# Kernel optimization log

Measured on AMD Instinct MI355X. Metric: run time of the kernel, lower is better.

## Reference

```python
import jax, jax.numpy as jnp
import numpy as np

EPS = 1e-12  # matches torch.nn.functional.normalize default eps


def setup_inputs() -> dict:
    key = jax.random.key(0)
    k1, k2 = jax.random.split(key)
    text_emb = jax.random.normal(k1, (64, 512), dtype=jnp.float32)
    spot_embs = jax.random.normal(k2, (500000, 512), dtype=jnp.float32)
    return {"text_emb": text_emb, "spot_embs": spot_embs, "top_k": 10}


def _l2_normalize(x):
    # F.normalize: x / max(||x||_2, eps)
    n = jnp.linalg.norm(x, axis=-1, keepdims=True)
    return x / jnp.maximum(n, EPS)


def reference(text_emb, spot_embs, top_k):
    t = _l2_normalize(text_emb)          # [B, D]
    s = _l2_normalize(spot_embs)         # [N, D]
    scores = jnp.einsum('bd,nd->bn', t, s)  # [B, N] cosine similarity
    _, indices = jax.lax.top_k(scores, top_k)  # [B, top_k]
    return scores, indices
```

## Files before the change

### kernel.cpp

```cpp
#include <hip/hip_runtime.h>
#include <hip/hip_bf16.h>

#define B_TEXT 64
#define D_DIM  512
#define TOPK   10
#define TILE_N 128
#define BK     64
#define LDA    (BK + 8)
#define CH     16

typedef short bf16x8 __attribute__((ext_vector_type(8)));
typedef float f32x4  __attribute__((ext_vector_type(4)));

__device__ __forceinline__ unsigned short f2bf(float x) {
    unsigned u = __float_as_uint(x);
    u += 0x7fffu + ((u >> 16) & 1u);
    return (unsigned short)(u >> 16);
}
__device__ __forceinline__ float bf2f(unsigned short h) {
    return __uint_as_float(((unsigned)h) << 16);
}

__global__ void prep_text(const float* __restrict__ T, unsigned short* __restrict__ tHi,
                          unsigned short* __restrict__ tLo) {
    int b = blockIdx.x;
    int lane = threadIdx.x;
    const float* row = T + b * D_DIM;
    float4 a = *(const float4*)(row + lane * 4);
    float4 c = *(const float4*)(row + 256 + lane * 4);
    float p = a.x*a.x + a.y*a.y + a.z*a.z + a.w*a.w
            + c.x*c.x + c.y*c.y + c.z*c.z + c.w*c.w;
    #pragma unroll
    for (int off = 1; off < 64; off <<= 1) p += __shfl_xor(p, off);
    float inv = 1.0f / fmaxf(sqrtf(p), 1e-12f);
    float v[8] = {a.x, a.y, a.z, a.w, c.x, c.y, c.z, c.w};
    #pragma unroll
    for (int j = 0; j < 8; ++j) {
        float y = v[j] * inv;
        unsigned short hi = f2bf(y);
        unsigned short lo = f2bf(y - bf2f(hi));
        int col = (j < 4) ? (lane * 4 + j) : (256 + lane * 4 + (j - 4));
        tHi[b * D_DIM + col] = hi;
        tLo[b * D_DIM + col] = lo;
    }
}

__global__ __launch_bounds__(256, 2) void gemm_scores(
    const float* __restrict__ S, const unsigned short* __restrict__ tHi,
    const unsigned short* __restrict__ tLo, float* __restrict__ out, int N) {

    __shared__ unsigned short As_hi[B_TEXT][LDA];
    __shared__ unsigned short As_lo[B_TEXT][LDA];
    __shared__ unsigned short Bs_hi[TILE_N][LDA];
    __shared__ unsigned short Bs_lo[TILE_N][LDA];
    __shared__ float s_ss[TILE_N];

    const int tid  = threadIdx.x;
    const int n0   = blockIdx.x * TILE_N;
    const int lane = tid & 63;
    const int w    = tid >> 6;
    const int l15  = lane & 15;
    const int quad = lane >> 4;

    if (tid < TILE_N) s_ss[tid] = 0.0f;

    f32x4 acc[4][2];
    const f32x4 zf = {0.f, 0.f, 0.f, 0.f};
    #pragma unroll
    for (int i = 0; i < 4; ++i)
        #pragma unroll
        for (int j = 0; j < 2; ++j) acc[i][j] = zf;

    const int arow = tid >> 2;
    const int akq  = (tid & 3) << 4;

    for (int kc = 0; kc < D_DIM; kc += BK) {
        __syncthreads();
        {
            const uint4* ph = (const uint4*)(tHi + arow * D_DIM + kc + akq);
            const uint4* pl = (const uint4*)(tLo + arow * D_DIM + kc + akq);
            uint4 h0 = ph[0], h1 = ph[1];
            uint4 l0 = pl[0], l1 = pl[1];
            *(uint4*)&As_hi[arow][akq]     = h0;
            *(uint4*)&As_hi[arow][akq + 8] = h1;
            *(uint4*)&As_lo[arow][akq]     = l0;
            *(uint4*)&As_lo[arow][akq + 8] = l1;
        }
        #pragma unroll
        for (int i = 0; i < 8; ++i) {
            int flat = i * 1024 + tid * 4;
            int r = flat >> 6;
            int k = flat & 63;
            float4 v;
            if (n0 + r < N) v = *(const float4*)(S + (size_t)(n0 + r) * D_DIM + kc + k);
            else            v = make_float4(0.f, 0.f, 0.f, 0.f);
            ushort4 h, l;
            h.x = f2bf(v.x); l.x = f2bf(v.x - bf2f(h.x));
            h.y = f2bf(v.y); l.y = f2bf(v.y - bf2f(h.y));
            h.z = f2bf(v.z); l.z = f2bf(v.z - bf2f(h.z));
            h.w = f2bf(v.w); l.w = f2bf(v.w - bf2f(h.w));
            *(ushort4*)&Bs_hi[r][k] = h;
            *(ushort4*)&Bs_lo[r][k] = l;
            float p = v.x*v.x + v.y*v.y + v.z*v.z + v.w*v.w;
            p += __shfl_xor(p, 1);
            p += __shfl_xor(p, 2);
            p += __shfl_xor(p, 4);
            p += __shfl_xor(p, 8);
            if ((tid & 15) == 0) s_ss[r] += p;
        }
        __syncthreads();
        #pragma unroll
        for (int ks = 0; ks < 2; ++ks) {
            const int off = ks * 32 + quad * 8;
            bf16x8 ah[4], al[4], bh[2], bl[2];
            #pragma unroll
            for (int mt = 0; mt < 4; ++mt) {
                int m = mt * 16 + l15;
                ah[mt] = *(const bf16x8*)&As_hi[m][off];
                al[mt] = *(const bf16x8*)&As_lo[m][off];
            }
            #pragma unroll
            for (int nt = 0; nt < 2; ++nt) {
                int nl = w * 32 + nt * 16 + l15;
                bh[nt] = *(const bf16x8*)&Bs_hi[nl][off];
                bl[nt] = *(const bf16x8*)&Bs_lo[nl][off];
            }
            #pragma unroll
            for (int mt = 0; mt < 4; ++mt)
                #pragma unroll
                for (int nt = 0; nt < 2; ++nt) {
                    acc[mt][nt] = __builtin_amdgcn_mfma_f32_16x16x32_bf16(ah[mt], bh[nt], acc[mt][nt], 0, 0, 0);
                    acc[mt][nt] = __builtin_amdgcn_mfma_f32_16x16x32_bf16(ah[mt], bl[nt], acc[mt][nt], 0, 0, 0);
                    acc[mt][nt] = __builtin_amdgcn_mfma_f32_16x16x32_bf16(al[mt], bh[nt], acc[mt][nt], 0, 0, 0);
                }
        }
    }
    __syncthreads();
    #pragma unroll
    for (int nt = 0; nt < 2; ++nt) {
        int nl = w * 32 + nt * 16 + l15;
        int n  = n0 + nl;
        if (n >= N) continue;
        float inv = 1.0f / fmaxf(sqrtf(s_ss[nl]), 1e-12f);
        #pragma unroll
        for (int mt = 0; mt < 4; ++mt) {
            #pragma unroll
            for (int r = 0; r < 4; ++r) {
                int m = mt * 16 + quad * 4 + r;
                out[(size_t)m * N + n] = acc[mt][nt][r] * inv;
            }
        }
    }
}

__global__ __launch_bounds__(256) void topk_part(
    const float* __restrict__ scores, float* __restrict__ cs, int* __restrict__ ci, int N) {
    const int b = blockIdx.y;
    const int c = blockIdx.x;
    const int t = threadIdx.x;
    const int chunk = (N + CH - 1) / CH;
    const int base  = c * chunk;
    const float* row = scores + (size_t)b * N;

    float ts[TOPK]; int ti[TOPK];
    #pragma unroll
    for (int j = 0; j < TOPK; ++j) { ts[j] = -3.4e38f; ti[j] = 0x7fffffff; }

    for (int e = t; e < chunk; e += 256) {
        int n = base + e;
        if (n >= N) break;
        float v = row[n];
        if (v > ts[TOPK - 1]) {
            float cv = v; int cidx = n;
            #pragma unroll
            for (int j = 0; j < TOPK; ++j) {
                bool g = (cv > ts[j]);
                float ns = g ? cv : ts[j]; int ni = g ? cidx : ti[j];
                cv = g ? ts[j] : cv; cidx = g ? ti[j] : cidx;
                ts[j] = ns; ti[j] = ni;
            }
        }
    }

    __shared__ float all_s[256][TOPK];
    __shared__ int   all_i[256][TOPK];
    #pragma unroll
    for (int j = 0; j < TOPK; ++j) { all_s[t][j] = ts[j]; all_i[t][j] = ti[j]; }

    __shared__ float rs[256]; __shared__ int ri[256]; __shared__ int rt[256];
    int ptr = 0;
    __syncthreads();

    for (int round = 0; round < TOPK; ++round) {
        rs[t] = (ptr < TOPK) ? all_s[t][ptr] : -3.4e38f;
        ri[t] = (ptr < TOPK) ? all_i[t][ptr] : 0x7fffffff;
        rt[t] = t;
        __syncthreads();
        for (int s = 128; s > 0; s >>= 1) {
            if (t < s) {
                bool take = (rs[t + s] > rs[t]) ||
                            (rs[t + s] == rs[t] && ri[t + s] < ri[t]);
                if (take) { rs[t] = rs[t + s]; ri[t] = ri[t + s]; rt[t] = rt[t + s]; }
            }
            __syncthreads();
        }
        if (t == 0) {
            cs[((size_t)b * CH + c) * TOPK + round] = rs[0];
            ci[((size_t)b * CH + c) * TOPK + round] = ri[0];
        }
        if (t == rt[0]) ++ptr;
        __syncthreads();
    }
}

__global__ void topk_final(const float* __restrict__ cs, const int* __restrict__ ci,
                           float* __restrict__ outIdx) {
    const int b = blockIdx.x;
    const int t = threadIdx.x;
    __shared__ float fs[CH * TOPK];
    __shared__ int   fi[CH * TOPK];
    for (int j = t; j < CH * TOPK; j += 64) {
        fs[j] = cs[(size_t)b * CH * TOPK + j];
        fi[j] = ci[(size_t)b * CH * TOPK + j];
    }
    __syncthreads();
    if (t == 0) {
        float ts[TOPK]; int ti[TOPK];
        #pragma unroll
        for (int j = 0; j < TOPK; ++j) { ts[j] = -3.4e38f; ti[j] = 0x7fffffff; }
        for (int e = 0; e < CH * TOPK; ++e) {
            float cv = fs[e]; int cidx = fi[e];
            if (cv > ts[TOPK - 1] || (cv == ts[TOPK - 1] && cidx < ti[TOPK - 1])) {
                #pragma unroll
                for (int j = 0; j < TOPK; ++j) {
                    bool g = (cv > ts[j]) || (cv == ts[j] && cidx < ti[j]);
                    float ns = g ? cv : ts[j]; int ni = g ? cidx : ti[j];
                    cv = g ? ts[j] : cv; cidx = g ? ti[j] : cidx;
                    ts[j] = ns; ti[j] = ni;
                }
            }
        }
        #pragma unroll
        for (int j = 0; j < TOPK; ++j) outIdx[b * TOPK + j] = (float)ti[j];
    }
}

extern "C" void kernel_launch(void* const* d_in, const int* in_sizes, int n_in,
                              void* d_out, int out_size, void* d_ws, size_t ws_size,
                              hipStream_t stream) {
    const float* T = (const float*)d_in[0];
    const float* S = (const float*)d_in[1];
    const int N = in_sizes[1] / D_DIM;
    float* out = (float*)d_out;

    unsigned short* tHi = (unsigned short*)d_ws;
    unsigned short* tLo = tHi + B_TEXT * D_DIM;
    float* cs = (float*)(tLo + B_TEXT * D_DIM);
    int*   ci = (int*)(cs + B_TEXT * CH * TOPK);

    prep_text<<<B_TEXT, 64, 0, stream>>>(T, tHi, tLo);
    int nblk = (N + TILE_N - 1) / TILE_N;
    gemm_scores<<<nblk, 256, 0, stream>>>(S, tHi, tLo, out, N);
    dim3 g3(CH, B_TEXT);
    topk_part<<<g3, 256, 0, stream>>>(out, cs, ci, N);
    topk_final<<<B_TEXT, 64, 0, stream>>>(cs, ci, out + (size_t)B_TEXT * N);
}
```

Before: 1.737 ms.

## Prefetch next K-tile into registers, swizzle LDS, vectorize top-k scan

The GEMM main loop now issues global loads for the next K-chunk before the MFMA work on the current one, then converts and stores them to LDS afterward, overlapping load latency with compute. The padded LDS arrays become an XOR-swizzled layout, which removes the padding and is meant to avoid bank conflicts. Sum-of-squares accumulation moves from shared-memory atomics-style updates into registers. Occupancy hint rises to 3 blocks per CU. The top-k partial scan reads float4 per thread with the chunk size rounded to a multiple of 4. Risks are higher register pressure from the prefetch buffers and an extra barrier per iteration.

```diff
diff --git a/kernel.cpp b/kernel.cpp
--- a/kernel.cpp
+++ b/kernel.cpp
@@ -1,12 +1,10 @@
 #include <hip/hip_runtime.h>
-#include <hip/hip_bf16.h>
 
 #define B_TEXT 64
 #define D_DIM  512
 #define TOPK   10
 #define TILE_N 128
 #define BK     64
-#define LDA    (BK + 8)
 #define CH     16
 
 typedef short bf16x8 __attribute__((ext_vector_type(8)));
@@ -19,6 +17,10 @@
 }
 __device__ __forceinline__ float bf2f(unsigned short h) {
     return __uint_as_float(((unsigned)h) << 16);
+}
+
+__device__ __forceinline__ int swz(int row, int k) {
+    return row * 64 + ((((k >> 3) ^ (row & 7)) << 3) | (k & 7));
 }
 
 __global__ void prep_text(const float* __restrict__ T, unsigned short* __restrict__ tHi,
@@ -45,14 +47,14 @@
     }
 }
 
-__global__ __launch_bounds__(256, 2) void gemm_scores(
+__global__ __launch_bounds__(256, 3) void gemm_scores(
     const float* __restrict__ S, const unsigned short* __restrict__ tHi,
     const unsigned short* __restrict__ tLo, float* __restrict__ out, int N) {
 
-    __shared__ unsigned short As_hi[B_TEXT][LDA];
-    __shared__ unsigned short As_lo[B_TEXT][LDA];
-    __shared__ unsigned short Bs_hi[TILE_N][LDA];
-    __shared__ unsigned short Bs_lo[TILE_N][LDA];
+    __shared__ __align__(16) unsigned short As_hi[B_TEXT * 64];
+    __shared__ __align__(16) unsigned short As_lo[B_TEXT * 64];
+    __shared__ __align__(16) unsigned short Bs_hi[TILE_N * 64];
+    __shared__ __align__(16) unsigned short Bs_lo[TILE_N * 64];
     __shared__ float s_ss[TILE_N];
 
     const int tid  = threadIdx.x;
@@ -62,7 +64,10 @@
     const int l15  = lane & 15;
     const int quad = lane >> 4;
 
-    if (tid < TILE_N) s_ss[tid] = 0.0f;
+    const int arow = tid >> 2;
+    const int akq  = (tid & 3) << 4;
+    const int bk   = (tid & 15) << 2;
+    const int br0  = tid >> 4;
 
     f32x4 acc[4][2];
     const f32x4 zf = {0.f, 0.f, 0.f, 0.f};
@@ -71,44 +76,69 @@
         #pragma unroll
         for (int j = 0; j < 2; ++j) acc[i][j] = zf;
 
-    const int arow = tid >> 2;
-    const int akq  = (tid & 3) << 4;
-
-    for (int kc = 0; kc < D_DIM; kc += BK) {
-        __syncthreads();
-        {
-            const uint4* ph = (const uint4*)(tHi + arow * D_DIM + kc + akq);
-            const uint4* pl = (const uint4*)(tLo + arow * D_DIM + kc + akq);
-            uint4 h0 = ph[0], h1 = ph[1];
-            uint4 l0 = pl[0], l1 = pl[1];
-            *(uint4*)&As_hi[arow][akq]     = h0;
-            *(uint4*)&As_hi[arow][akq + 8] = h1;
-            *(uint4*)&As_lo[arow][akq]     = l0;
-            *(uint4*)&As_lo[arow][akq + 8] = l1;
-        }
+    float ssq[8];
+    #pragma unroll
+    for (int i = 0; i < 8; ++i) ssq[i] = 0.0f;
+
+    float4 bv[8];
+    uint4 a_h0, a_h1, a_l0, a_l1;
+    ushort4 hh[8], ll[8];
+
+    auto issue = [&](int kc) {
+        const uint4* ph = (const uint4*)(tHi + arow * D_DIM + kc + akq);
+        const uint4* pl = (const uint4*)(tLo + arow * D_DIM + kc + akq);
+        a_h0 = ph[0]; a_h1 = ph[1];
+        a_l0 = pl[0]; a_l1 = pl[1];
+        const float* sp = S + (size_t)(n0 + br0) * D_DIM + kc + bk;
         #pragma unroll
         for (int i = 0; i < 8; ++i) {
-            int flat = i * 1024 + tid * 4;
-            int r = flat >> 6;
-            int k = flat & 63;
-            float4 v;
-            if (n0 + r < N) v = *(const float4*)(S + (size_t)(n0 + r) * D_DIM + kc + k);
-            else            v = make_float4(0.f, 0.f, 0.f, 0.f);
+            int r = i * 16 + br0;
+            if (n0 + r < N) bv[i] = *(const float4*)(sp + (size_t)i * 16 * D_DIM);
+            else            bv[i] = make_float4(0.f, 0.f, 0.f, 0.f);
+        }
+    };
+
+    auto convert = [&]() {
+        #pragma unroll
+        for (int i = 0; i < 8; ++i) {
+            float4 v = bv[i];
             ushort4 h, l;
             h.x = f2bf(v.x); l.x = f2bf(v.x - bf2f(h.x));
             h.y = f2bf(v.y); l.y = f2bf(v.y - bf2f(h.y));
             h.z = f2bf(v.z); l.z = f2bf(v.z - bf2f(h.z));
             h.w = f2bf(v.w); l.w = f2bf(v.w - bf2f(h.w));
-            *(ushort4*)&Bs_hi[r][k] = h;
-            *(ushort4*)&Bs_lo[r][k] = l;
+            hh[i] = h; ll[i] = l;
             float p = v.x*v.x + v.y*v.y + v.z*v.z + v.w*v.w;
             p += __shfl_xor(p, 1);
             p += __shfl_xor(p, 2);
             p += __shfl_xor(p, 4);
             p += __shfl_xor(p, 8);
-            if ((tid & 15) == 0) s_ss[r] += p;
-        }
-        __syncthreads();
+            ssq[i] += p;
+        }
+    };
+
+    auto stage_write = [&]() {
+        *(uint4*)&As_hi[swz(arow, akq)]     = a_h0;
+        *(uint4*)&As_hi[swz(arow, akq + 8)] = a_h1;
+        *(uint4*)&As_lo[swz(arow, akq)]     = a_l0;
+        *(uint4*)&As_lo[swz(arow, akq + 8)] = a_l1;
+        #pragma unroll
+        for (int i = 0; i < 8; ++i) {
+            int r = i * 16 + br0;
+            *(ushort4*)&Bs_hi[swz(r, bk)] = hh[i];
+            *(ushort4*)&Bs_lo[swz(r, bk)] = ll[i];
+        }
+    };
+
+    issue(0);
+    convert();
+    stage_write();
+    __syncthreads();
+
+    for (int kc = 0; kc < D_DIM; kc += BK) {
+        const bool more = (kc + BK) < D_DIM;
+        if (more) issue(kc + BK);
+
         #pragma unroll
         for (int ks = 0; ks < 2; ++ks) {
             const int off = ks * 32 + quad * 8;
@@ -116,14 +146,14 @@
             #pragma unroll
             for (int mt = 0; mt < 4; ++mt) {
                 int m = mt * 16 + l15;
-                ah[mt] = *(const bf16x8*)&As_hi[m][off];
-                al[mt] = *(const bf16x8*)&As_lo[m][off];
+                ah[mt] = *(const bf16x8*)&As_hi[swz(m, off)];
+                al[mt] = *(const bf16x8*)&As_lo[swz(m, off)];
             }
             #pragma unroll
             for (int nt = 0; nt < 2; ++nt) {
                 int nl = w * 32 + nt * 16 + l15;
-                bh[nt] = *(const bf16x8*)&Bs_hi[nl][off];
-                bl[nt] = *(const bf16x8*)&Bs_lo[nl][off];
+                bh[nt] = *(const bf16x8*)&Bs_hi[swz(nl, off)];
+                bl[nt] = *(const bf16x8*)&Bs_lo[swz(nl, off)];
             }
             #pragma unroll
             for (int mt = 0; mt < 4; ++mt)
@@ -134,8 +164,21 @@
                     acc[mt][nt] = __builtin_amdgcn_mfma_f32_16x16x32_bf16(al[mt], bh[nt], acc[mt][nt], 0, 0, 0);
                 }
         }
+
+        if (more) {
+            convert();
+            __syncthreads();
+            stage_write();
+            __syncthreads();
+        }
+    }
+
+    if ((tid & 15) == 0) {
+        #pragma unroll
+        for (int i = 0; i < 8; ++i) s_ss[i * 16 + br0] = ssq[i];
     }
     __syncthreads();
+
     #pragma unroll
     for (int nt = 0; nt < 2; ++nt) {
         int nl = w * 32 + nt * 16 + l15;
@@ -158,7 +201,7 @@
     const int b = blockIdx.y;
     const int c = blockIdx.x;
     const int t = threadIdx.x;
-    const int chunk = (N + CH - 1) / CH;
+    const int chunk = (((N + CH - 1) / CH) + 3) & ~3;
     const int base  = c * chunk;
     const float* row = scores + (size_t)b * N;
 
@@ -166,18 +209,31 @@
     #pragma unroll
     for (int j = 0; j < TOPK; ++j) { ts[j] = -3.4e38f; ti[j] = 0x7fffffff; }
 
-    for (int e = t; e < chunk; e += 256) {
+    for (int e = t * 4; e < chunk; e += 1024) {
         int n = base + e;
         if (n >= N) break;
-        float v = row[n];
-        if (v > ts[TOPK - 1]) {
-            float cv = v; int cidx = n;
-            #pragma unroll
-            for (int j = 0; j < TOPK; ++j) {
-                bool g = (cv > ts[j]);
-                float ns = g ? cv : ts[j]; int ni = g ? cidx : ti[j];
-                cv = g ? ts[j] : cv; cidx = g ? ti[j] : cidx;
-                ts[j] = ns; ti[j] = ni;
+        float4 v4;
+        if (n + 3 < N) {
+            v4 = *(const float4*)(row + n);
+        } else {
+            v4.x = row[n];
+            v4.y = (n + 1 < N) ? row[n + 1] : -3.4e38f;
+            v4.z = (n + 2 < N) ? row[n + 2] : -3.4e38f;
+            v4.w = (n + 3 < N) ? row[n + 3] : -3.4e38f;
+        }
+        float vv[4] = {v4.x, v4.y, v4.z, v4.w};
+        #pragma unroll
+        for (int q = 0; q < 4; ++q) {
+            float v = vv[q];
+            if (v > ts[TOPK - 1]) {
+                float cv = v; int cidx = n + q;
+                #pragma unroll
+                for (int j = 0; j < TOPK; ++j) {
+                    bool g = (cv > ts[j]);
+                    float ns = g ? cv : ts[j]; int ni = g ? cidx : ti[j];
+                    cv = g ? ts[j] : cv; cidx = g ? ti[j] : cidx;
+                    ts[j] = ns; ti[j] = ni;
+                }
             }
         }
     }
```

Result: faster. 1.507 ms (-13.2%).
